# Optimization experiments

Hardware: AMD Instinct MI355X
Metric: run time of the kernel (lower is better)

The kernel has to match this reference:

```python
import jax, jax.numpy as jnp
import numpy as np

C = 256
GROUPS = 32
EPS = 1e-5

def setup_inputs() -> dict:
    key = jax.random.key(0)
    ks = jax.random.split(key, 7)
    B, H, W = 4, 64, 64
    x = jax.random.normal(ks[0], (B, C, H, W), dtype=jnp.float32)
    # GroupNorm affine params
    gn_w = jnp.ones((C,), dtype=jnp.float32)
    gn_b = jnp.zeros((C,), dtype=jnp.float32)
    # 1x1 conv weights stored as [out, in]
    s = 1.0 / np.sqrt(C)
    qkv_w = jax.random.uniform(ks[1], (3 * C, C), minval=-s, maxval=s, dtype=jnp.float32)
    qkv_b = jax.random.uniform(ks[2], (3 * C,), minval=-s, maxval=s, dtype=jnp.float32)
    proj_w = jax.random.uniform(ks[3], (C, C), minval=-s, maxval=s, dtype=jnp.float32)
    proj_b = jax.random.uniform(ks[4], (C,), minval=-s, maxval=s, dtype=jnp.float32)
    return {"x": x, "gn_w": gn_w, "gn_b": gn_b, "qkv_w": qkv_w,
            "qkv_b": qkv_b, "proj_w": proj_w, "proj_b": proj_b}

def group_norm(x, w, b):
    B, Cc, H, W = x.shape
    xg = x.reshape(B, GROUPS, Cc // GROUPS, H, W)
    mu = xg.mean(axis=(2, 3, 4), keepdims=True)
    var = xg.var(axis=(2, 3, 4), keepdims=True)
    xn = ((xg - mu) * jax.lax.rsqrt(var + EPS)).reshape(B, Cc, H, W)
    return xn * w[None, :, None, None] + b[None, :, None, None]

def reference(x, gn_w, gn_b, qkv_w, qkv_b, proj_w, proj_b):
    B, Cc, H, W = x.shape
    h = group_norm(x, gn_w, gn_b)
    # 1x1 conv == per-pixel matmul
    qkv = jnp.einsum('bchw,oc->bohw', h, qkv_w) + qkv_b[None, :, None, None]
    q, k, v = jnp.split(qkv, 3, axis=1)            # each [B, C, H, W]
    N = H * W
    q = q.reshape(B, Cc, N).transpose(0, 2, 1)      # [B, N, C]
    k = k.reshape(B, Cc, N)                         # [B, C, N]
    v = v.reshape(B, Cc, N).transpose(0, 2, 1)      # [B, N, C]
    w_att = jnp.einsum('bnc,bcm->bnm', q, k) * (Cc ** -0.5)
    w_att = jax.nn.softmax(w_att, axis=-1)
    h = jnp.einsum('bnm,bmc->bnc', w_att, v)        # [B, N, C]
    h = h.transpose(0, 2, 1).reshape(B, Cc, H, W)
    h = jnp.einsum('bchw,oc->bohw', h, proj_w) + proj_b[None, :, None, None]
    return x + h
```

## Files before the change

kernel.cpp:

```cpp
#include <hip/hip_runtime.h>
#include <stdint.h>

typedef unsigned short u16;
typedef __attribute__((ext_vector_type(8))) short bf16x8;
typedef __attribute__((ext_vector_type(4))) float f32x4;

#define BATCH   4
#define CH      256
#define NPIX    4096
#define NGROUPS 32
#define CPG     8
#define EPS     1e-5f

#define NSPLIT 4
#define SPLEN  (NPIX / NSPLIT)
#define ATK    32
#define NIT    (SPLEN / ATK)
#define KSTR   264
#define VSTR   40
#define WSTR   264

__device__ __forceinline__ float bf2f(u16 u) {
    union { uint32_t i; float f; } v; v.i = ((uint32_t)u) << 16; return v.f;
}
__device__ __forceinline__ u16 f2bf(float f) {
    union { float f; uint32_t i; } v; v.f = f;
    uint32_t x = v.i;
    uint32_t r = (x + 0x7fffu + ((x >> 16) & 1u)) >> 16;
    return (u16)r;
}
__device__ __forceinline__ void unpack2(uint32_t u, float& a, float& b) {
    union { uint32_t i; float f; } lo, hi;
    lo.i = u << 16; hi.i = u & 0xffff0000u;
    a = lo.f; b = hi.f;
}
__device__ __forceinline__ void unpack8(uint4 u, float* f) {
    unpack2(u.x, f[0], f[1]); unpack2(u.y, f[2], f[3]);
    unpack2(u.z, f[4], f[5]); unpack2(u.w, f[6], f[7]);
}

__device__ __forceinline__ bool detect_f32(const void* xv) {
    const u16* p = (const u16*)xv;
    int bad = 0;
    #pragma unroll
    for (int i = 0; i < 32; i++) {
        u16 v = p[2 * i];
        int e = (v >> 7) & 0xff;
        bad += (e < 0x68 || e > 0x90) ? 1 : 0;
    }
    return bad >= 10;
}
__device__ __forceinline__ float load1(const void* b, size_t i, bool f32) {
    return f32 ? ((const float*)b)[i] : bf2f(((const u16*)b)[i]);
}
__device__ __forceinline__ void store1(void* b, size_t i, bool f32, float v) {
    if (f32) ((float*)b)[i] = v; else ((u16*)b)[i] = f2bf(v);
}
__device__ __forceinline__ void load4v(const void* base, size_t off, bool f32, float* f) {
    if (f32) {
        float4 a = *(const float4*)((const float*)base + off);
        f[0] = a.x; f[1] = a.y; f[2] = a.z; f[3] = a.w;
    } else {
        uint2 u = *(const uint2*)((const u16*)base + off);
        unpack2(u.x, f[0], f[1]); unpack2(u.y, f[2], f[3]);
    }
}
__device__ __forceinline__ void load8v(const void* base, size_t off, bool f32, float* f) {
    if (f32) {
        const float4* p = (const float4*)((const float*)base + off);
        float4 a = p[0], b = p[1];
        f[0] = a.x; f[1] = a.y; f[2] = a.z; f[3] = a.w;
        f[4] = b.x; f[5] = b.y; f[6] = b.z; f[7] = b.w;
    } else {
        uint4 u = *(const uint4*)((const u16*)base + off);
        unpack8(u, f);
    }
}

__global__ __launch_bounds__(256) void wconv(const void* __restrict__ qkv_w,
                                             const void* __restrict__ proj_w,
                                             u16* __restrict__ wq, u16* __restrict__ wp) {
    bool f32q = detect_f32(qkv_w);
    bool f32p = detect_f32(proj_w);
    int i = blockIdx.x * 256 + threadIdx.x;
    for (int e = i; e < 768 * 256; e += 256 * 256)
        wq[e] = f2bf(load1(qkv_w, e, f32q));
    for (int e = i; e < 256 * 256; e += 256 * 256)
        wp[e] = f2bf(load1(proj_w, e, f32p));
}

__global__ __launch_bounds__(256) void gn_stats(const void* __restrict__ x,
                                                float* __restrict__ stats, int b0) {
    bool f32 = detect_f32(x);
    int bg = b0 * NGROUPS + blockIdx.x;
    int t  = threadIdx.x;
    size_t base = (size_t)bg * (CPG * NPIX);
    float s = 0.f, s2 = 0.f;
    for (int i = t * 8; i < CPG * NPIX; i += 256 * 8) {
        float f[8]; load8v(x, base + i, f32, f);
        #pragma unroll
        for (int e = 0; e < 8; e++) { s += f[e]; s2 += f[e] * f[e]; }
    }
    #pragma unroll
    for (int off = 1; off < 64; off <<= 1) {
        s  += __shfl_xor(s,  off);
        s2 += __shfl_xor(s2, off);
    }
    __shared__ float red[8];
    int w = t >> 6;
    if ((t & 63) == 0) { red[w * 2] = s; red[w * 2 + 1] = s2; }
    __syncthreads();
    if (t == 0) {
        float S  = red[0] + red[2] + red[4] + red[6];
        float S2 = red[1] + red[3] + red[5] + red[7];
        float n  = (float)(CPG * NPIX);
        float mu = S / n;
        float var = S2 / n - mu * mu;
        stats[bg * 2]     = mu;
        stats[bg * 2 + 1] = rsqrtf(var + EPS);
    }
}

__global__ __launch_bounds__(256) void xgn(const void* __restrict__ x,
                                           const void* __restrict__ gn_w,
                                           const void* __restrict__ gn_b,
                                           const float* __restrict__ stats,
                                           u16* __restrict__ xt, int b0) {
    bool f32 = detect_f32(x);
    __shared__ u16 T[64][72];
    int bl = blockIdx.z, bg = b0 + bl;
    int n0 = blockIdx.x * 64, c0 = blockIdx.y * 64;
    int t = threadIdx.x;
    int tc = t >> 4, tn = (t & 15) * 4;
    #pragma unroll
    for (int i = 0; i < 4; i++) {
        int cl = tc + i * 16;
        int c = c0 + cl;
        int g = c >> 3;
        float mu = stats[(bg * NGROUPS + g) * 2];
        float rs = stats[(bg * NGROUPS + g) * 2 + 1];
        float wv = load1(gn_w, c, f32) * rs;
        float bv = load1(gn_b, c, f32) - mu * wv;
        float a[4];
        load4v(x, ((size_t)(bg * CH + c)) * NPIX + n0 + tn, f32, a);
        #pragma unroll
        for (int j = 0; j < 4; j++) T[cl][tn + j] = f2bf(a[j] * wv + bv);
    }
    __syncthreads();
    #pragma unroll
    for (int i = 0; i < 2; i++) {
        int e = t + i * 256;
        int nl = e >> 3, cc = (e & 7) * 8;
        union { uint4 v; u16 s[8]; } pk;
        #pragma unroll
        for (int j = 0; j < 8; j++) pk.s[j] = T[cc + j][nl];
        *(uint4*)(xt + ((size_t)(bl * NPIX) + n0 + nl) * CH + c0 + cc) = pk.v;
    }
}

__global__ __launch_bounds__(256, 4) void qkv_mfma(const u16* __restrict__ xt,
                                                   const u16* __restrict__ wq,
                                                   const void* __restrict__ qkv_b,
                                                   u16* __restrict__ qk,
                                                   u16* __restrict__ vt) {
    __shared__ u16 Ws[64 * WSTR];
    bool f32b = detect_f32(qkv_b);
    int bl = blockIdx.z;
    int n0 = blockIdx.x * 128, o0 = blockIdx.y * 64;
    int t = threadIdx.x;
    int w = t >> 6, lane = t & 63;
    int l15 = lane & 15, quad = lane >> 4;
    int pbase = n0 + w * 32;

    #pragma unroll
    for (int i = 0; i < 8; i++) {
        int e = t + i * 256;
        *(uint4*)(Ws + (e >> 5) * WSTR + (e & 31) * 8) =
            *(const uint4*)(wq + (size_t)(o0 + (e >> 5)) * CH + (e & 31) * 8);
    }
    __syncthreads();

    const u16* xa = xt + ((size_t)(bl * NPIX + pbase)) * CH;
    f32x4 acc[2][4];
    #pragma unroll
    for (int m = 0; m < 2; m++)
        #pragma unroll
        for (int n = 0; n < 4; n++)
            #pragma unroll
            for (int r = 0; r < 4; r++) acc[m][n][r] = 0.f;

    #pragma unroll
    for (int kc = 0; kc < 8; kc++) {
        bf16x8 a0 = *(const bf16x8*)(xa + (size_t)(l15) * CH + kc * 32 + quad * 8);
        bf16x8 a1 = *(const bf16x8*)(xa + (size_t)(16 + l15) * CH + kc * 32 + quad * 8);
        #pragma unroll
        for (int n = 0; n < 4; n++) {
            bf16x8 b = *(const bf16x8*)(Ws + (n * 16 + l15) * WSTR + kc * 32 + quad * 8);
            acc[0][n] = __builtin_amdgcn_mfma_f32_16x16x32_bf16(a0, b, acc[0][n], 0, 0, 0);
            acc[1][n] = __builtin_amdgcn_mfma_f32_16x16x32_bf16(a1, b, acc[1][n], 0, 0, 0);
        }
    }

    bool isv = (o0 >= 512);
    if (!isv) {
        u16* T2 = Ws;
        __syncthreads();
        #pragma unroll
        for (int n = 0; n < 4; n++) {
            int o = o0 + n * 16 + l15;
            float bias = load1(qkv_b, o, f32b);
            #pragma unroll
            for (int m = 0; m < 2; m++)
                #pragma unroll
                for (int r = 0; r < 4; r++) {
                    int prow = w * 32 + m * 16 + quad * 4 + r;
                    T2[prow * 72 + n * 16 + l15] = f2bf(acc[m][n][r] + bias);
                }
        }
        __syncthreads();
        #pragma unroll
        for (int i = 0; i < 4; i++) {
            int e = t + i * 256;
            int p = e >> 3, c = (e & 7) * 8;
            uint4 v = *(const uint4*)(T2 + p * 72 + c);
            *(uint4*)(qk + ((size_t)(bl * NPIX + n0 + p)) * 512 + o0 + c) = v;
        }
    } else {
        #pragma unroll
        for (int n = 0; n < 4; n++) {
            int o = o0 + n * 16 + l15;
            float bias = load1(qkv_b, o, f32b);
            size_t rowb = ((size_t)(bl * CH + o - 512)) * NPIX + pbase;
            #pragma unroll
            for (int m = 0; m < 2; m++) {
                union { uint2 v; u16 s[4]; } pk;
                #pragma unroll
                for (int r = 0; r < 4; r++) pk.s[r] = f2bf(acc[m][n][r] + bias);
                *(uint2*)(vt + rowb + quad * 8 + m * 4) = pk.v;
            }
        }
    }
}

__global__ __launch_bounds__(256, 2) void attn_mfma(const u16* __restrict__ qk,
                                                    const u16* __restrict__ vt,
                                                    u16* __restrict__ Opart,
                                                    float* __restrict__ lpart,
                                                    int NE, int NR) {
    __shared__ u16 Ks[ATK * KSTR];
    __shared__ u16 Vts[CH * VSTR];
    int bl    = blockIdx.z;
    int split = blockIdx.y;
    int q0    = blockIdx.x * 128;
    int t     = threadIdx.x;
    int w     = t >> 6, lane = t & 63;
    int l15   = lane & 15, quad = lane >> 4;

    const u16* qkb = qk + (size_t)bl * NPIX * 512;
    const u16* vtb = vt + (size_t)bl * CH * NPIX;
    int kvbase = split * SPLEN;

    bf16x8 qf[2][8];
    #pragma unroll
    for (int m = 0; m < 2; m++) {
        const u16* qrow = qkb + (size_t)(q0 + w * 32 + m * 16 + l15) * 512;
        #pragma unroll
        for (int kc = 0; kc < 8; kc++)
            qf[m][kc] = *(const bf16x8*)(qrow + kc * 32 + quad * 8);
    }
    f32x4 o[2][16];
    #pragma unroll
    for (int m = 0; m < 2; m++)
        #pragma unroll
        for (int i = 0; i < 16; i++)
            #pragma unroll
            for (int r = 0; r < 4; r++) o[m][i][r] = 0.f;
    float lsum[2] = {0.f, 0.f};
    const float scale = 0.0625f;

    for (int it = 0; it < NIT; it++) {
        int kv0 = kvbase + it * ATK;
        __syncthreads();
        #pragma unroll
        for (int i = 0; i < 4; i++) {
            int e = t + i * 256;
            *(uint4*)(Ks + (e >> 5) * KSTR + (e & 31) * 8) =
                *(const uint4*)(qkb + (size_t)(kv0 + (e >> 5)) * 512 + 256 + (e & 31) * 8);
        }
        #pragma unroll
        for (int i = 0; i < 4; i++) {
            int e = t + i * 256;
            *(uint4*)(Vts + (e >> 2) * VSTR + (e & 3) * 8) =
                *(const uint4*)(vtb + (size_t)(e >> 2) * NPIX + kv0 + (e & 3) * 8);
        }
        __syncthreads();

        f32x4 sT[2][2];
        #pragma unroll
        for (int kt = 0; kt < 2; kt++)
            #pragma unroll
            for (int qt = 0; qt < 2; qt++)
                #pragma unroll
                for (int r = 0; r < 4; r++) sT[kt][qt][r] = 0.f;
        #pragma unroll
        for (int kc = 0; kc < 8; kc++) {
            bf16x8 a0 = *(const bf16x8*)(Ks + l15 * KSTR + kc * 32 + quad * 8);
            bf16x8 a1 = *(const bf16x8*)(Ks + (16 + l15) * KSTR + kc * 32 + quad * 8);
            sT[0][0] = __builtin_amdgcn_mfma_f32_16x16x32_bf16(a0, qf[0][kc], sT[0][0], 0, 0, 0);
            sT[0][1] = __builtin_amdgcn_mfma_f32_16x16x32_bf16(a0, qf[1][kc], sT[0][1], 0, 0, 0);
            sT[1][0] = __builtin_amdgcn_mfma_f32_16x16x32_bf16(a1, qf[0][kc], sT[1][0], 0, 0, 0);
            sT[1][1] = __builtin_amdgcn_mfma_f32_16x16x32_bf16(a1, qf[1][kc], sT[1][1], 0, 0, 0);
        }

        bf16x8 pa[2];
        #pragma unroll
        for (int qt = 0; qt < 2; qt++) {
            union { bf16x8 v; u16 s[8]; } pk;
            float ls = 0.f;
            #pragma unroll
            for (int kt = 0; kt < 2; kt++)
                #pragma unroll
                for (int r = 0; r < 4; r++) {
                    float p = __expf(sT[kt][qt][r] * scale);
                    ls += p;
                    pk.s[kt * 4 + r] = f2bf(p);
                }
            lsum[qt] += ls;
            pa[qt] = pk.v;
        }

        #pragma unroll
        for (int dt = 0; dt < 16; dt++) {
            bf16x8 vf = *(const bf16x8*)(Vts + (dt * 16 + l15) * VSTR + quad * 8);
            o[0][dt] = __builtin_amdgcn_mfma_f32_16x16x32_bf16(pa[0], vf, o[0][dt], 0, 0, 0);
            o[1][dt] = __builtin_amdgcn_mfma_f32_16x16x32_bf16(pa[1], vf, o[1][dt], 0, 0, 0);
        }
    }

    size_t rowb = (size_t)bl * NPIX + q0 + w * 32;
    u16* op = Opart + (size_t)split * NE;
    #pragma unroll
    for (int qt = 0; qt < 2; qt++) {
        float v = lsum[qt];
        v += __shfl_xor(v, 16); v += __shfl_xor(v, 32);
        if (quad == 0)
            lpart[(size_t)split * NR + rowb + qt * 16 + l15] = v;
        #pragma unroll
        for (int dt = 0; dt < 16; dt++)
            #pragma unroll
            for (int r = 0; r < 4; r++)
                op[(rowb + qt * 16 + quad * 4 + r) * CH + dt * 16 + l15] = f2bf(o[qt][dt][r]);
    }
}

__global__ __launch_bounds__(256, 4) void proj_mfma(const u16* __restrict__ Opart,
                                                    const float* __restrict__ lpart,
                                                    const u16* __restrict__ wp,
                                                    const void* __restrict__ proj_b,
                                                    const void* __restrict__ x,
                                                    void* __restrict__ out,
                                                    int b0, int NE, int NR) {
    __shared__ u16 Ws[64 * WSTR];
    bool f32 = detect_f32(x);
    int bl = blockIdx.z, bg = b0 + bl;
    int n0 = blockIdx.x * 128, o0 = blockIdx.y * 64;
    int t = threadIdx.x;
    int w = t >> 6, lane = t & 63;
    int l15 = lane & 15, quad = lane >> 4;
    int pbase = n0 + w * 32;

    #pragma unroll
    for (int i = 0; i < 8; i++) {
        int e = t + i * 256;
        *(uint4*)(Ws + (e >> 5) * WSTR + (e & 31) * 8) =
            *(const uint4*)(wp + (size_t)(o0 + (e >> 5)) * CH + (e & 31) * 8);
    }
    __syncthreads();

    size_t rowg[2]; float invl[2];
    #pragma unroll
    for (int m = 0; m < 2; m++) {
        rowg[m] = (size_t)bl * NPIX + pbase + m * 16 + l15;
        float l = 0.f;
        #pragma unroll
        for (int s = 0; s < NSPLIT; s++) l += lpart[(size_t)s * NR + rowg[m]];
        invl[m] = 1.0f / l;
    }

    f32x4 acc[2][4];
    #pragma unroll
    for (int m = 0; m < 2; m++)
        #pragma unroll
        for (int n = 0; n < 4; n++)
            #pragma unroll
            for (int r = 0; r < 4; r++) acc[m][n][r] = 0.f;

    #pragma unroll
    for (int kc = 0; kc < 8; kc++) {
        bf16x8 afr[2];
        #pragma unroll
        for (int m = 0; m < 2; m++) {
            float f[8] = {0.f,0.f,0.f,0.f,0.f,0.f,0.f,0.f};
            #pragma unroll
            for (int s = 0; s < NSPLIT; s++) {
                bf16x8 v = *(const bf16x8*)(Opart + (size_t)s * NE + rowg[m] * CH + kc * 32 + quad * 8);
                #pragma unroll
                for (int j = 0; j < 8; j++) f[j] += bf2f((u16)v[j]);
            }
            bf16x8 a;
            #pragma unroll
            for (int j = 0; j < 8; j++) a[j] = (short)f2bf(f[j] * invl[m]);
            afr[m] = a;
        }
        #pragma unroll
        for (int n = 0; n < 4; n++) {
            bf16x8 b = *(const bf16x8*)(Ws + (n * 16 + l15) * WSTR + kc * 32 + quad * 8);
            acc[0][n] = __builtin_amdgcn_mfma_f32_16x16x32_bf16(afr[0], b, acc[0][n], 0, 0, 0);
            acc[1][n] = __builtin_amdgcn_mfma_f32_16x16x32_bf16(afr[1], b, acc[1][n], 0, 0, 0);
        }
    }

    __syncthreads();
    float4* T4 = (float4*)Ws;
    #pragma unroll
    for (int n = 0; n < 4; n++) {
        int o = o0 + n * 16 + l15;
        float bias = load1(proj_b, o, f32);
        #pragma unroll
        for (int m = 0; m < 2; m++) {
            float4 v;
            v.x = acc[m][n][0] + bias; v.y = acc[m][n][1] + bias;
            v.z = acc[m][n][2] + bias; v.w = acc[m][n][3] + bias;
            T4[(n * 16 + l15) * 33 + w * 8 + m * 4 + quad] = v;
        }
    }
    __syncthreads();
    const float* Tf = (const float*)Ws;
    if (f32) {
        #pragma unroll
        for (int i = 0; i < 8; i++) {
            int idx = t + i * 256;
            int row = idx >> 5, c4 = idx & 31;
            float4 v = T4[row * 33 + c4];
            size_t go = ((size_t)(bg * CH + o0 + row)) * NPIX + n0 + c4 * 4;
            float4 xr = *(const float4*)((const float*)x + go);
            v.x += xr.x; v.y += xr.y; v.z += xr.z; v.w += xr.w;
            *(float4*)((float*)out + go) = v;
        }
    } else {
        #pragma unroll
        for (int i = 0; i < 4; i++) {
            int idx = t + i * 256;
            int row = idx >> 4, c8 = idx & 15;
            size_t go = ((size_t)(bg * CH + o0 + row)) * NPIX + n0 + c8 * 8;
            uint4 xr = *(const uint4*)((const u16*)x + go);
            float xf[8]; unpack8(xr, xf);
            union { uint4 v; u16 s[8]; } pk;
            #pragma unroll
            for (int j = 0; j < 8; j++)
                pk.s[j] = f2bf(Tf[row * 132 + c8 * 8 + j] + xf[j]);
            *(uint4*)((u16*)out + go) = pk.v;
        }
    }
}

extern "C" void kernel_launch(void* const* d_in, const int* in_sizes, int n_in,
                              void* d_out, int out_size, void* d_ws, size_t ws_size,
                              hipStream_t stream) {
    const void* x      = d_in[0];
    const void* gn_w   = d_in[1];
    const void* gn_b   = d_in[2];
    const void* qkv_w  = d_in[3];
    const void* qkv_b  = d_in[4];
    const void* proj_w = d_in[5];
    const void* proj_b = d_in[6];

    char* ws = (char*)d_ws;
    float* stats = (float*)ws;
    u16* wq = (u16*)(ws + 1024);
    u16* wp = wq + 768 * 256;
    char* dyn = ws + 1024 + (768 * 256 + 256 * 256) * 2;

    const size_t per_batch = (size_t)NPIX * CH * 2
                           + (size_t)NPIX * 512 * 2
                           + (size_t)CH * NPIX * 2
                           + (size_t)NSPLIT * NPIX * CH * 2
                           + (size_t)NSPLIT * NPIX * 4;
    const size_t need_full = 1024 + 600 * 1024 + BATCH * per_batch;
    int nb = (ws_size >= need_full) ? BATCH : 1;

    u16* xt      = (u16*)dyn;
    u16* qk      = xt + (size_t)nb * NPIX * CH;
    u16* vt      = qk + (size_t)nb * NPIX * 512;
    u16* Opart   = vt + (size_t)nb * CH * NPIX;
    float* lpart = (float*)(Opart + (size_t)NSPLIT * nb * NPIX * CH);
    int NE = nb * NPIX * CH;
    int NR = nb * NPIX;

    wconv<<<dim3(256), 256, 0, stream>>>(qkv_w, proj_w, wq, wp);

    for (int b0 = 0; b0 < BATCH; b0 += nb) {
        gn_stats<<<dim3(nb * NGROUPS), 256, 0, stream>>>(x, stats, b0);
        xgn<<<dim3(NPIX / 64, CH / 64, nb), 256, 0, stream>>>(
            x, gn_w, gn_b, stats, xt, b0);
        qkv_mfma<<<dim3(NPIX / 128, 768 / 64, nb), 256, 0, stream>>>(
            xt, wq, qkv_b, qk, vt);
        attn_mfma<<<dim3(NPIX / 128, NSPLIT, nb), 256, 0, stream>>>(
            qk, vt, Opart, lpart, NE, NR);
        proj_mfma<<<dim3(NPIX / 128, CH / 64, nb), 256, 0, stream>>>(
            Opart, lpart, wp, proj_b, x, d_out, b0, NE, NR);
    }
}
```

Before: 212.8 us.

## Double-buffer K/V tiles in LDS with register prefetch in attention kernel

Adds two LDS buffers for the K and V tiles and stages the next tiles through registers. Global loads for tile it+2 are issued during compute on tile it, and the store of tile it+1 into the alternate buffer happens at the start of each iteration. This replaces the two barriers per iteration with one and hides global-load latency behind the MFMA work. The costs are double the LDS (about 70KB per block, which may strain the two-blocks-per-CU launch bound) and 32 extra VGPRs for the staged data on top of a large accumulator array.

```diff
diff --git a/kernel.cpp b/kernel.cpp
--- a/kernel.cpp
+++ b/kernel.cpp
@@ -247,8 +247,8 @@
                                                     u16* __restrict__ Opart,
                                                     float* __restrict__ lpart,
                                                     int NE, int NR) {
-    __shared__ u16 Ks[ATK * KSTR];
-    __shared__ u16 Vts[CH * VSTR];
+    __shared__ u16 Ks[2][ATK * KSTR];
+    __shared__ u16 Vts[2][CH * VSTR];
     int bl    = blockIdx.z;
     int split = blockIdx.y;
     int q0    = blockIdx.x * 128;
@@ -278,22 +278,41 @@
     float lsum[2] = {0.f, 0.f};
     const float scale = 0.0625f;
 
+    uint4 kst[4], vst[4];
+    #pragma unroll
+    for (int i = 0; i < 4; i++) {
+        int e = t + i * 256;
+        kst[i] = *(const uint4*)(qkb + (size_t)(kvbase + (e >> 5)) * 512 + 256 + (e & 31) * 8);
+        vst[i] = *(const uint4*)(vtb + (size_t)(e >> 2) * NPIX + kvbase + (e & 3) * 8);
+    }
+    #pragma unroll
+    for (int i = 0; i < 4; i++) {
+        int e = t + i * 256;
+        *(uint4*)(&Ks[0][(e >> 5) * KSTR + (e & 31) * 8]) = kst[i];
+        *(uint4*)(&Vts[0][(e >> 2) * VSTR + (e & 3) * 8]) = vst[i];
+    }
+    #pragma unroll
+    for (int i = 0; i < 4; i++) {
+        int e = t + i * 256;
+        kst[i] = *(const uint4*)(qkb + (size_t)(kvbase + ATK + (e >> 5)) * 512 + 256 + (e & 31) * 8);
+        vst[i] = *(const uint4*)(vtb + (size_t)(e >> 2) * NPIX + kvbase + ATK + (e & 3) * 8);
+    }
+    __syncthreads();
+
     for (int it = 0; it < NIT; it++) {
-        int kv0 = kvbase + it * ATK;
-        __syncthreads();
-        #pragma unroll
-        for (int i = 0; i < 4; i++) {
-            int e = t + i * 256;
-            *(uint4*)(Ks + (e >> 5) * KSTR + (e & 31) * 8) =
-                *(const uint4*)(qkb + (size_t)(kv0 + (e >> 5)) * 512 + 256 + (e & 31) * 8);
-        }
-        #pragma unroll
-        for (int i = 0; i < 4; i++) {
-            int e = t + i * 256;
-            *(uint4*)(Vts + (e >> 2) * VSTR + (e & 3) * 8) =
-                *(const uint4*)(vtb + (size_t)(e >> 2) * NPIX + kv0 + (e & 3) * 8);
-        }
-        __syncthreads();
+        int cur = it & 1;
+        if (it + 1 < NIT) {
+            u16* KsB = &Ks[cur ^ 1][0];
+            u16* VsB = &Vts[cur ^ 1][0];
+            #pragma unroll
+            for (int i = 0; i < 4; i++) {
+                int e = t + i * 256;
+                *(uint4*)(KsB + (e >> 5) * KSTR + (e & 31) * 8) = kst[i];
+                *(uint4*)(VsB + (e >> 2) * VSTR + (e & 3) * 8) = vst[i];
+            }
+        }
+        const u16* KsC = &Ks[cur][0];
+        const u16* VsC = &Vts[cur][0];
 
         f32x4 sT[2][2];
         #pragma unroll
@@ -304,8 +323,8 @@
                 for (int r = 0; r < 4; r++) sT[kt][qt][r] = 0.f;
         #pragma unroll
         for (int kc = 0; kc < 8; kc++) {
-            bf16x8 a0 = *(const bf16x8*)(Ks + l15 * KSTR + kc * 32 + quad * 8);
-            bf16x8 a1 = *(const bf16x8*)(Ks + (16 + l15) * KSTR + kc * 32 + quad * 8);
+            bf16x8 a0 = *(const bf16x8*)(KsC + l15 * KSTR + kc * 32 + quad * 8);
+            bf16x8 a1 = *(const bf16x8*)(KsC + (16 + l15) * KSTR + kc * 32 + quad * 8);
             sT[0][0] = __builtin_amdgcn_mfma_f32_16x16x32_bf16(a0, qf[0][kc], sT[0][0], 0, 0, 0);
             sT[0][1] = __builtin_amdgcn_mfma_f32_16x16x32_bf16(a0, qf[1][kc], sT[0][1], 0, 0, 0);
             sT[1][0] = __builtin_amdgcn_mfma_f32_16x16x32_bf16(a1, qf[0][kc], sT[1][0], 0, 0, 0);
@@ -329,12 +348,24 @@
             pa[qt] = pk.v;
         }
 
+        if (it + 2 < NIT) {
+            int kv2 = kvbase + (it + 2) * ATK;
+            #pragma unroll
+            for (int i = 0; i < 4; i++) {
+                int e = t + i * 256;
+                kst[i] = *(const uint4*)(qkb + (size_t)(kv2 + (e >> 5)) * 512 + 256 + (e & 31) * 8);
+                vst[i] = *(const uint4*)(vtb + (size_t)(e >> 2) * NPIX + kv2 + (e & 3) * 8);
+            }
+        }
+
         #pragma unroll
         for (int dt = 0; dt < 16; dt++) {
-            bf16x8 vf = *(const bf16x8*)(Vts + (dt * 16 + l15) * VSTR + quad * 8);
+            bf16x8 vf = *(const bf16x8*)(VsC + (dt * 16 + l15) * VSTR + quad * 8);
             o[0][dt] = __builtin_amdgcn_mfma_f32_16x16x32_bf16(pa[0], vf, o[0][dt], 0, 0, 0);
             o[1][dt] = __builtin_amdgcn_mfma_f32_16x16x32_bf16(pa[1], vf, o[1][dt], 0, 0, 0);
         }
+
+        __syncthreads();
     }
 
     size_t rowb = (size_t)bl * NPIX + q0 + w * 32;
```

Result: slower. 338.5 us (+59.0%).

## Use direct global-to-LDS loads with XOR swizzle in attention; reuse weights across two QKV tiles

Applied to the files above, without the earlier changes.

The attention kernel now stages K and V tiles with global_load_lds, which copies straight from global memory into LDS without a register round trip. K uses an XOR swizzle in place of padded rows to avoid bank conflicts, and V drops its padding. The QKV projection block now loops over two pixel tiles so each weight tile loaded into LDS is reused twice, using a separate LDS staging buffer and a lower occupancy bound. The risks are bank conflicts on the unpadded V reads and fewer QKV blocks in flight.

```diff
diff --git a/kernel.cpp b/kernel.cpp
--- a/kernel.cpp
+++ b/kernel.cpp
@@ -16,9 +16,8 @@
 #define SPLEN  (NPIX / NSPLIT)
 #define ATK    32
 #define NIT    (SPLEN / ATK)
-#define KSTR   264
-#define VSTR   40
 #define WSTR   264
+#define QTILES 2
 
 __device__ __forceinline__ float bf2f(u16 u) {
     union { uint32_t i; float f; } v; v.i = ((uint32_t)u) << 16; return v.f;
@@ -158,19 +157,19 @@
     }
 }
 
-__global__ __launch_bounds__(256, 4) void qkv_mfma(const u16* __restrict__ xt,
+__global__ __launch_bounds__(256, 3) void qkv_mfma(const u16* __restrict__ xt,
                                                    const u16* __restrict__ wq,
                                                    const void* __restrict__ qkv_b,
                                                    u16* __restrict__ qk,
                                                    u16* __restrict__ vt) {
     __shared__ u16 Ws[64 * WSTR];
+    __shared__ u16 T2b[128 * 72];
     bool f32b = detect_f32(qkv_b);
     int bl = blockIdx.z;
-    int n0 = blockIdx.x * 128, o0 = blockIdx.y * 64;
+    int o0 = blockIdx.y * 64;
     int t = threadIdx.x;
     int w = t >> 6, lane = t & 63;
     int l15 = lane & 15, quad = lane >> 4;
-    int pbase = n0 + w * 32;
 
     #pragma unroll
     for (int i = 0; i < 8; i++) {
@@ -180,63 +179,67 @@
     }
     __syncthreads();
 
-    const u16* xa = xt + ((size_t)(bl * NPIX + pbase)) * CH;
-    f32x4 acc[2][4];
-    #pragma unroll
-    for (int m = 0; m < 2; m++)
-        #pragma unroll
-        for (int n = 0; n < 4; n++)
-            #pragma unroll
-            for (int r = 0; r < 4; r++) acc[m][n][r] = 0.f;
-
-    #pragma unroll
-    for (int kc = 0; kc < 8; kc++) {
-        bf16x8 a0 = *(const bf16x8*)(xa + (size_t)(l15) * CH + kc * 32 + quad * 8);
-        bf16x8 a1 = *(const bf16x8*)(xa + (size_t)(16 + l15) * CH + kc * 32 + quad * 8);
-        #pragma unroll
-        for (int n = 0; n < 4; n++) {
-            bf16x8 b = *(const bf16x8*)(Ws + (n * 16 + l15) * WSTR + kc * 32 + quad * 8);
-            acc[0][n] = __builtin_amdgcn_mfma_f32_16x16x32_bf16(a0, b, acc[0][n], 0, 0, 0);
-            acc[1][n] = __builtin_amdgcn_mfma_f32_16x16x32_bf16(a1, b, acc[1][n], 0, 0, 0);
-        }
-    }
-
     bool isv = (o0 >= 512);
-    if (!isv) {
-        u16* T2 = Ws;
-        __syncthreads();
-        #pragma unroll
-        for (int n = 0; n < 4; n++) {
-            int o = o0 + n * 16 + l15;
-            float bias = load1(qkv_b, o, f32b);
-            #pragma unroll
-            for (int m = 0; m < 2; m++)
+    for (int tt = 0; tt < QTILES; tt++) {
+        int n0 = (blockIdx.x * QTILES + tt) * 128;
+        int pbase = n0 + w * 32;
+        const u16* xa = xt + ((size_t)(bl * NPIX + pbase)) * CH;
+
+        f32x4 acc[2][4];
+        #pragma unroll
+        for (int m = 0; m < 2; m++)
+            #pragma unroll
+            for (int n = 0; n < 4; n++)
                 #pragma unroll
-                for (int r = 0; r < 4; r++) {
-                    int prow = w * 32 + m * 16 + quad * 4 + r;
-                    T2[prow * 72 + n * 16 + l15] = f2bf(acc[m][n][r] + bias);
+                for (int r = 0; r < 4; r++) acc[m][n][r] = 0.f;
+
+        #pragma unroll
+        for (int kc = 0; kc < 8; kc++) {
+            bf16x8 a0 = *(const bf16x8*)(xa + (size_t)(l15) * CH + kc * 32 + quad * 8);
+            bf16x8 a1 = *(const bf16x8*)(xa + (size_t)(16 + l15) * CH + kc * 32 + quad * 8);
+            #pragma unroll
+            for (int n = 0; n < 4; n++) {
+                bf16x8 b = *(const bf16x8*)(Ws + (n * 16 + l15) * WSTR + kc * 32 + quad * 8);
+                acc[0][n] = __builtin_amdgcn_mfma_f32_16x16x32_bf16(a0, b, acc[0][n], 0, 0, 0);
+                acc[1][n] = __builtin_amdgcn_mfma_f32_16x16x32_bf16(a1, b, acc[1][n], 0, 0, 0);
+            }
+        }
+
+        if (!isv) {
+            __syncthreads();
+            #pragma unroll
+            for (int n = 0; n < 4; n++) {
+                int o = o0 + n * 16 + l15;
+                float bias = load1(qkv_b, o, f32b);
+                #pragma unroll
+                for (int m = 0; m < 2; m++)
+                    #pragma unroll
+                    for (int r = 0; r < 4; r++) {
+                        int prow = w * 32 + m * 16 + quad * 4 + r;
+                        T2b[prow * 72 + n * 16 + l15] = f2bf(acc[m][n][r] + bias);
+                    }
+            }
+            __syncthreads();
+            #pragma unroll
+            for (int i = 0; i < 4; i++) {
+                int e = t + i * 256;
+                int p = e >> 3, c = (e & 7) * 8;
+                uint4 v = *(const uint4*)(T2b + p * 72 + c);
+                *(uint4*)(qk + ((size_t)(bl * NPIX + n0 + p)) * 512 + o0 + c) = v;
+            }
+        } else {
+            #pragma unroll
+            for (int n = 0; n < 4; n++) {
+                int o = o0 + n * 16 + l15;
+                float bias = load1(qkv_b, o, f32b);
+                size_t rowb = ((size_t)(bl * CH + o - 512)) * NPIX + pbase;
+                #pragma unroll
+                for (int m = 0; m < 2; m++) {
+                    union { uint2 v; u16 s[4]; } pk;
+                    #pragma unroll
+                    for (int r = 0; r < 4; r++) pk.s[r] = f2bf(acc[m][n][r] + bias);
+                    *(uint2*)(vt + rowb + quad * 8 + m * 4) = pk.v;
                 }
-        }
-        __syncthreads();
-        #pragma unroll
-        for (int i = 0; i < 4; i++) {
-            int e = t + i * 256;
-            int p = e >> 3, c = (e & 7) * 8;
-            uint4 v = *(const uint4*)(T2 + p * 72 + c);
-            *(uint4*)(qk + ((size_t)(bl * NPIX + n0 + p)) * 512 + o0 + c) = v;
-        }
-    } else {
-        #pragma unroll
-        for (int n = 0; n < 4; n++) {
-            int o = o0 + n * 16 + l15;
-            float bias = load1(qkv_b, o, f32b);
-            size_t rowb = ((size_t)(bl * CH + o - 512)) * NPIX + pbase;
-            #pragma unroll
-            for (int m = 0; m < 2; m++) {
-                union { uint2 v; u16 s[4]; } pk;
-                #pragma unroll
-                for (int r = 0; r < 4; r++) pk.s[r] = f2bf(acc[m][n][r] + bias);
-                *(uint2*)(vt + rowb + quad * 8 + m * 4) = pk.v;
             }
         }
     }
@@ -247,8 +250,8 @@
                                                     u16* __restrict__ Opart,
                                                     float* __restrict__ lpart,
                                                     int NE, int NR) {
-    __shared__ u16 Ks[ATK * KSTR];
-    __shared__ u16 Vts[CH * VSTR];
+    __shared__ u16 Ks[ATK * 256];
+    __shared__ u16 Vts[CH * 32];
     int bl    = blockIdx.z;
     int split = blockIdx.y;
     int q0    = blockIdx.x * 128;
@@ -277,21 +280,26 @@
             for (int r = 0; r < 4; r++) o[m][i][r] = 0.f;
     float lsum[2] = {0.f, 0.f};
     const float scale = 0.0625f;
+    int swz = l15 & 7;
 
     for (int it = 0; it < NIT; it++) {
         int kv0 = kvbase + it * ATK;
         __syncthreads();
         #pragma unroll
         for (int i = 0; i < 4; i++) {
-            int e = t + i * 256;
-            *(uint4*)(Ks + (e >> 5) * KSTR + (e & 31) * 8) =
-                *(const uint4*)(qkb + (size_t)(kv0 + (e >> 5)) * 512 + 256 + (e & 31) * 8);
+            int g = t + i * 256;
+            int row = g >> 5, pcol = g & 31;
+            int lcol = pcol ^ (row & 7);
+            __builtin_amdgcn_global_load_lds(
+                (const void*)(qkb + (size_t)(kv0 + row) * 512 + 256 + lcol * 8),
+                (void*)(Ks + (size_t)g * 8), 16, 0, 0);
         }
         #pragma unroll
         for (int i = 0; i < 4; i++) {
-            int e = t + i * 256;
-            *(uint4*)(Vts + (e >> 2) * VSTR + (e & 3) * 8) =
-                *(const uint4*)(vtb + (size_t)(e >> 2) * NPIX + kv0 + (e & 3) * 8);
+            int g = t + i * 256;
+            __builtin_amdgcn_global_load_lds(
+                (const void*)(vtb + (size_t)(g >> 2) * NPIX + kv0 + (g & 3) * 8),
+                (void*)(Vts + (size_t)g * 8), 16, 0, 0);
         }
         __syncthreads();
 
@@ -304,8 +312,9 @@
                 for (int r = 0; r < 4; r++) sT[kt][qt][r] = 0.f;
         #pragma unroll
         for (int kc = 0; kc < 8; kc++) {
-            bf16x8 a0 = *(const bf16x8*)(Ks + l15 * KSTR + kc * 32 + quad * 8);
-            bf16x8 a1 = *(const bf16x8*)(Ks + (16 + l15) * KSTR + kc * 32 + quad * 8);
+            int sc = (kc * 4 + quad) ^ swz;
+            bf16x8 a0 = *(const bf16x8*)(Ks + l15 * 256 + sc * 8);
+            bf16x8 a1 = *(const bf16x8*)(Ks + (16 + l15) * 256 + sc * 8);
             sT[0][0] = __builtin_amdgcn_mfma_f32_16x16x32_bf16(a0, qf[0][kc], sT[0][0], 0, 0, 0);
             sT[0][1] = __builtin_amdgcn_mfma_f32_16x16x32_bf16(a0, qf[1][kc], sT[0][1], 0, 0, 0);
             sT[1][0] = __builtin_amdgcn_mfma_f32_16x16x32_bf16(a1, qf[0][kc], sT[1][0], 0, 0, 0);
@@ -331,7 +340,7 @@
 
         #pragma unroll
         for (int dt = 0; dt < 16; dt++) {
-            bf16x8 vf = *(const bf16x8*)(Vts + (dt * 16 + l15) * VSTR + quad * 8);
+            bf16x8 vf = *(const bf16x8*)(Vts + (dt * 16 + l15) * 32 + quad * 8);
             o[0][dt] = __builtin_amdgcn_mfma_f32_16x16x32_bf16(pa[0], vf, o[0][dt], 0, 0, 0);
             o[1][dt] = __builtin_amdgcn_mfma_f32_16x16x32_bf16(pa[1], vf, o[1][dt], 0, 0, 0);
         }
@@ -503,7 +512,7 @@
         gn_stats<<<dim3(nb * NGROUPS), 256, 0, stream>>>(x, stats, b0);
         xgn<<<dim3(NPIX / 64, CH / 64, nb), 256, 0, stream>>>(
             x, gn_w, gn_b, stats, xt, b0);
-        qkv_mfma<<<dim3(NPIX / 128, 768 / 64, nb), 256, 0, stream>>>(
+        qkv_mfma<<<dim3(NPIX / 128 / QTILES, 768 / 64, nb), 256, 0, stream>>>(
             xt, wq, qkv_b, qk, vt);
         attn_mfma<<<dim3(NPIX / 128, NSPLIT, nb), 256, 0, stream>>>(
             qk, vt, Opart, lpart, NE, NR);
```

After: 208.9 us. Within noise of the previous version (-1.8%).
